# Kernel tuning notes

Measured on AMD Instinct MI355X. Metric: run time of the kernel, lower is better.

## Reference

```python
import jax, jax.numpy as jnp
import numpy as np

R_MAX = 10.0
NUM_BESSEL = 8
POLY_P = 5
EMB = 64
MLP_DIM = 256
NUM_LAYERS = 3
IN_DIM = 10
OUT_DIM = 1
N_NODES = 256
N_EDGES = 1024
N_GRAPHS = 16
# gated TP output: 0e channel carries 64 scalars + 128 gates (one per gated 1o/2e irrep)
GATE_MUL = {0: 3 * EMB, 1: EMB, 2: EMB}
L0_PATHS = [(0, 0, 0), (0, 1, 1), (0, 2, 2)]  # in_irreps = 64x0e
LN_PATHS = [(0, 0, 0), (1, 1, 0), (2, 2, 0), (0, 1, 1), (1, 0, 1), (1, 2, 1), (2, 1, 1), (0, 2, 2), (2, 0, 2), (1, 1, 2), (2, 2, 2)]

def _npaths(paths):
    d = {0: 0, 1: 0, 2: 0}
    for _, _, l3 in paths:
        d[l3] += 1
    return d

L0_NP = _npaths(L0_PATHS)
LN_NP = _npaths(LN_PATHS)
L0_NUMEL = sum(EMB * GATE_MUL[l3] for _, _, l3 in L0_PATHS)   # 20480
LN_NUMEL = sum(EMB * GATE_MUL[l3] for _, _, l3 in LN_PATHS)   # 69632

# ---- real spherical harmonics, component normalization (||Y_l||^2 = 2l+1) ----
def _sh_np(v):
    x, y, z = v[:, 0], v[:, 1], v[:, 2]
    s15 = np.sqrt(15.0)
    return {0: np.ones((v.shape[0], 1)),
            1: np.sqrt(3.0) * np.stack([x, y, z], 1),
            2: np.stack([s15 * x * y, s15 * y * z, 0.5 * np.sqrt(5.0) * (3 * z * z - 1), s15 * x * z, 0.5 * s15 * (x * x - y * y)], 1)}

def _rot(axis, t):
    c, s = np.cos(t), np.sin(t)
    R = np.eye(3)
    i, j = [(1, 2), (2, 0), (0, 1)][axis]
    R[i, i] = c; R[j, j] = c; R[i, j] = -s; R[j, i] = s
    return R

_PTS = np.random.RandomState(0).randn(64, 3)
_PTS /= np.linalg.norm(_PTS, axis=1, keepdims=True)

def _D(l, R):
    # rep matrix D with Y(Rv) = D @ Y(v), fit by least squares over sample points
    A = _sh_np(_PTS)[l]
    B = _sh_np(_PTS @ R.T)[l]
    return np.linalg.lstsq(A, B, rcond=None)[0].T

def _gen(l, axis, eps=1e-4):
    return (_D(l, _rot(axis, eps)) - _D(l, _rot(axis, -eps))) / (2 * eps)

def _cg(l1, l2, l3):
    # Clebsch-Gordan tensor as null space of the infinitesimal equivariance constraint
    d1, d2, d3 = 2 * l1 + 1, 2 * l2 + 1, 2 * l3 + 1
    rows = []
    for a in range(3):
        J1, J2, J3 = _gen(l1, a), _gen(l2, a), _gen(l3, a)
        rows.append(np.kron(J1.T, np.eye(d2 * d3)) + np.kron(np.eye(d1), np.kron(J2.T, np.eye(d3))) - np.kron(np.eye(d1 * d2), J3))
    _, _, Vh = np.linalg.svd(np.vstack(rows))
    c = Vh[-1].reshape(d1, d2, d3)
    c = c / np.linalg.norm(c)
    c = c * np.sign(c.flat[int(np.argmax(np.abs(c)))])
    return c

CG = {p: jnp.asarray(_cg(*p), jnp.float32) for p in set(LN_PATHS)}

def _sh_jax(u):
    x, y, z = u[..., 0], u[..., 1], u[..., 2]
    s15 = 15.0 ** 0.5
    return {0: jnp.ones_like(x)[:, None],
            1: (3.0 ** 0.5) * jnp.stack([x, y, z], -1),
            2: jnp.stack([s15 * x * y, s15 * y * z, 0.5 * (5.0 ** 0.5) * (3 * z * z - 1), s15 * x * z, 0.5 * s15 * (x * x - y * y)], -1)}

def _radial(r):
    # Bessel radial basis * polynomial cutoff envelope (MACE-style RadialEmbeddingBlock)
    n = jnp.arange(1, NUM_BESSEL + 1, dtype=r.dtype)
    bessel = (2.0 / R_MAX) ** 0.5 * jnp.sin(n * jnp.pi * r[:, None] / R_MAX) / r[:, None]
    x = r / R_MAX
    p = POLY_P
    env = 1.0 - 0.5 * (p + 1) * (p + 2) * x ** p + p * (p + 2) * x ** (p + 1) - 0.5 * p * (p + 1) * x ** (p + 2)
    env = env * (x < 1.0)
    return bessel * env[:, None]

def _conv(h, sh, ef, recv, send, paths, n_per, w1, b1, w2, b2):
    # TensorProductConvLayer: MLP(edge_feats) -> TP weights, CG tensor product, scatter-sum, gate
    E = ef.shape[0]
    w = jax.nn.relu(ef @ w1 + b1) @ w2 + b2  # (E, weight_numel)
    msgs = {0: 0.0, 1: 0.0, 2: 0.0}
    off = 0
    for (l1, l2, l3) in paths:
        mv = GATE_MUL[l3]
        wp = w[:, off:off + EMB * mv].reshape(E, EMB, mv)
        off += EMB * mv
        tmp = jnp.einsum('eui,ej,ijk->euk', h[l1][send], sh[l2], CG[(l1, l2, l3)])
        alpha = float(1.0 / np.sqrt(EMB * n_per[l3]))  # fan-in path normalization
        msgs[l3] = msgs[l3] + alpha * jnp.einsum('euk,euv->evk', tmp, wp)
    agg = {l: jax.ops.segment_sum(msgs[l], recv, num_segments=N_NODES) for l in msgs}
    s = agg[0][..., 0]  # (N, 192): 64 scalars + 128 gates
    return {0: jax.nn.silu(s[:, :EMB])[:, :, None],
            1: agg[1] * jax.nn.sigmoid(s[:, EMB:2 * EMB])[:, :, None],
            2: agg[2] * jax.nn.sigmoid(s[:, 2 * EMB:])[:, :, None]}

def _forward(atoms, pos, edge_index, batch, emb, l0_fc1_w, l0_fc1_b, l0_fc2_w, l0_fc2_b, fcs1_w, fcs1_b, fcs2_w, fcs2_b, pred_w1, pred_b1, pred_w2, pred_b2):
    recv, send = edge_index[0], edge_index[1]
    vec = pos[recv] - pos[send]
    r = jnp.maximum(jnp.linalg.norm(vec, axis=-1), 1e-6)
    sh = _sh_jax(vec / r[:, None])
    ef = _radial(r)
    h = {0: emb[atoms][:, :, None]}  # (N, 64, 1) scalar features
    h_new = _conv(h, sh, ef, recv, send, L0_PATHS, L0_NP, l0_fc1_w, l0_fc1_b, l0_fc2_w, l0_fc2_b)
    h_new[0] = h_new[0] + h[0]  # residual; F.pad means only scalar block overlaps
    h = h_new
    for i in range(NUM_LAYERS - 1):
        h_new = _conv(h, sh, ef, recv, send, LN_PATHS, LN_NP, fcs1_w[i], fcs1_b[i], fcs2_w[i], fcs2_b[i])
        h = {l: h_new[l] + h[l] for l in h_new}
    pooled = jax.ops.segment_sum(h[0][..., 0], batch, num_segments=N_GRAPHS)  # out[:, :emb_dim]
    return jax.nn.relu(pooled @ pred_w1 + pred_b1) @ pred_w2 + pred_b2

def setup_inputs():
    key = jax.random.key(0)
    ks = jax.random.split(key, 12)
    def lin(k, fi, fo):
        return jax.random.normal(k, (fi, fo), jnp.float32) * float(1.0 / np.sqrt(fi))
    return dict(
        atoms=jax.random.randint(ks[0], (N_NODES,), 0, IN_DIM),
        pos=jax.random.normal(ks[1], (N_NODES, 3), jnp.float32) * 2.0,
        edge_index=jax.random.randint(ks[2], (2, N_EDGES), 0, N_NODES),
        batch=jnp.sort(jax.random.randint(ks[3], (N_NODES,), 0, N_GRAPHS)),
        emb=jax.random.normal(ks[4], (IN_DIM, EMB), jnp.float32),
        l0_fc1_w=lin(ks[5], NUM_BESSEL, MLP_DIM), l0_fc1_b=jnp.zeros((MLP_DIM,), jnp.float32),
        l0_fc2_w=lin(ks[6], MLP_DIM, L0_NUMEL), l0_fc2_b=jnp.zeros((L0_NUMEL,), jnp.float32),
        fcs1_w=jax.random.normal(ks[7], (NUM_LAYERS - 1, NUM_BESSEL, MLP_DIM), jnp.float32) * float(1.0 / np.sqrt(NUM_BESSEL)),
        fcs1_b=jnp.zeros((NUM_LAYERS - 1, MLP_DIM), jnp.float32),
        fcs2_w=jax.random.normal(ks[8], (NUM_LAYERS - 1, MLP_DIM, LN_NUMEL), jnp.float32) * float(1.0 / np.sqrt(MLP_DIM)),
        fcs2_b=jnp.zeros((NUM_LAYERS - 1, LN_NUMEL), jnp.float32),
        pred_w1=lin(ks[9], EMB, EMB), pred_b1=jnp.zeros((EMB,), jnp.float32),
        pred_w2=lin(ks[10], EMB, OUT_DIM), pred_b2=jnp.zeros((OUT_DIM,), jnp.float32),
    )

def reference(atoms, pos, edge_index, batch, emb, l0_fc1_w, l0_fc1_b, l0_fc2_w, l0_fc2_b, fcs1_w, fcs1_b, fcs2_w, fcs2_b, pred_w1, pred_b1, pred_w2, pred_b2):
    return _forward(atoms, pos, edge_index, batch, emb, l0_fc1_w, l0_fc1_b, l0_fc2_w, l0_fc2_b, fcs1_w, fcs1_b, fcs2_w, fcs2_b, pred_w1, pred_b1, pred_w2, pred_b2)
```

## Files before the change

kernel.cpp:

```cpp
#include <hip/hip_runtime.h>
#include <hip/hip_bf16.h>
#include <math.h>

#define NE 1024
#define NN 256
#define NG 16
#define EMB 64
#define KD 256
#define BK 64
#define NUMEL_L0 20480
#define NUMEL_LN 69632
#define MSGW 704
#define MAXE 256

typedef __attribute__((ext_vector_type(8))) __bf16 bf16x8;
typedef __attribute__((ext_vector_type(4))) float f32x4;
typedef __attribute__((ext_vector_type(4))) unsigned int u32x4;

__device__ __align__(16) float g_sh[NE * 8];
__device__ __align__(16) float g_ef[NE * 8];
__device__ __align__(16) unsigned short g_hidb[NE * KD];
__device__ __align__(16) unsigned short g_w2t[(size_t)NUMEL_LN * KD];
__device__ __align__(16) unsigned short g_wb[(size_t)NE * NUMEL_LN];
__device__ __align__(16) float g_msgs[NE * MSGW];
__device__ __align__(16) float g_h0[NN * EMB];
__device__ __align__(16) float g_h1[NN * EMB * 3];
__device__ __align__(16) float g_h2[NN * EMB * 5];
__device__ int g_elist[NN * MAXE];
__device__ int g_ecnt[NN];
__device__ __align__(16) float g_pool[NG * EMB];
__device__ float g_cg[363];

__device__ __forceinline__ unsigned short f2b(float x) {
    __hip_bfloat16 h = __float2bfloat16(x);
    return *(unsigned short*)&h;
}
__device__ __forceinline__ float b2f(unsigned short u) {
    __hip_bfloat16 h;
    *(unsigned short*)&h = u;
    return __bfloat162float(h);
}

__device__ __forceinline__ void gld16(const void* g, void* l) {
    __builtin_amdgcn_global_load_lds(
        (const __attribute__((address_space(1))) unsigned int*)g,
        (__attribute__((address_space(3))) unsigned int*)l, 16, 0, 0);
}

struct Path { int l1, l2, d1, d2, d3, mv, off, cgoff, tmpoff; };

__constant__ Path PLN[11] = {
    {0, 0, 1, 1, 1, 192, 0,     0,   0},
    {1, 1, 3, 3, 1, 192, 12288, 1,   64},
    {2, 2, 5, 5, 1, 192, 24576, 10,  128},
    {0, 1, 1, 3, 3, 64,  36864, 35,  192},
    {1, 0, 3, 1, 3, 64,  40960, 44,  384},
    {1, 2, 3, 5, 3, 64,  45056, 53,  576},
    {2, 1, 5, 3, 3, 64,  49152, 98,  768},
    {0, 2, 1, 5, 5, 64,  53248, 143, 960},
    {2, 0, 5, 1, 5, 64,  57344, 168, 1280},
    {1, 1, 3, 3, 5, 64,  61440, 193, 1600},
    {2, 2, 5, 5, 5, 64,  65536, 238, 1920},
};
__constant__ Path PL0[3] = {
    {0, 0, 1, 1, 1, 192, 0,     0,   0},
    {0, 1, 1, 3, 3, 64,  12288, 35,  64},
    {0, 2, 1, 5, 5, 64,  16384, 143, 256},
};

__global__ void k_init_cg() {
    if (threadIdx.x != 0 || blockIdx.x != 0) return;
    for (int i = 0; i < 363; i++) g_cg[i] = 0.f;
    const float K3 = 0.57735026918962576f;
    const float K5 = 0.44721359549995794f;
    const float A  = 0.31622776601683794f;
    const float B  = 0.18257418583505536f;
    const float C2 = 0.36514837167011072f;
    const float P  = 0.23904572186687872f;
    const float Q  = 0.20701966780270626f;
    const float S  = 0.11952286093343936f;
    g_cg[0] = 1.f;
    for (int i = 0; i < 3; i++) g_cg[1 + i * 3 + i] = K3;
    for (int i = 0; i < 5; i++) g_cg[10 + i * 5 + i] = K5;
    for (int i = 0; i < 3; i++) g_cg[35 + i * 3 + i] = K3;
    for (int i = 0; i < 3; i++) g_cg[44 + i * 3 + i] = K3;
    g_cg[53 + 1]  = A;  g_cg[53 + 15] = A;  g_cg[53 + 20] = A;
    g_cg[53 + 34] = A;  g_cg[53 + 11] = A;  g_cg[53 + 39] = A;
    g_cg[53 + 6]  = -B; g_cg[53 + 22] = -B; g_cg[53 + 38] = C2;
    g_cg[53 + 12] = A;  g_cg[53 + 28] = -A;
    g_cg[98 + 1]  = A;  g_cg[98 + 3]  = A;  g_cg[98 + 14] = A;
    g_cg[98 + 16] = A;  g_cg[98 + 29] = A;  g_cg[98 + 33] = A;
    g_cg[98 + 18] = -B; g_cg[98 + 22] = -B; g_cg[98 + 26] = C2;
    g_cg[98 + 36] = A;  g_cg[98 + 40] = -A;
    for (int i = 0; i < 5; i++) g_cg[143 + i * 5 + i] = K5;
    for (int i = 0; i < 5; i++) g_cg[168 + i * 5 + i] = K5;
    g_cg[193 + 5]  = A;  g_cg[193 + 15] = A;  g_cg[193 + 26] = A;
    g_cg[193 + 36] = A;  g_cg[193 + 13] = A;  g_cg[193 + 33] = A;
    g_cg[193 + 2]  = -B; g_cg[193 + 22] = -B; g_cg[193 + 42] = C2;
    g_cg[193 + 4]  = A;  g_cg[193 + 24] = -A;
    g_cg[238 + 2]   = P;  g_cg[238 + 10]  = P;  g_cg[238 + 50]  = P;
    g_cg[238 + 8]   = -Q; g_cg[238 + 16]  = -Q; g_cg[238 + 28]  = -Q;
    g_cg[238 + 40]  = -Q; g_cg[238 + 76]  = -Q; g_cg[238 + 80]  = -Q;
    g_cg[238 + 32]  = -S; g_cg[238 + 36]  = -S; g_cg[238 + 56]  = -S;
    g_cg[238 + 34]  = Q;  g_cg[238 + 46]  = Q;  g_cg[238 + 106] = Q;
    g_cg[238 + 62]  = -P;
    g_cg[238 + 74]  = P;  g_cg[238 + 114] = P;  g_cg[238 + 122] = P;
    g_cg[238 + 68]  = -S; g_cg[238 + 88]  = -S; g_cg[238 + 92]  = -S;
    g_cg[238 + 94]  = -Q; g_cg[238 + 98]  = -Q; g_cg[238 + 118] = -Q;
}

__global__ void k_geom(const int* ei, const float* pos) {
    int e = blockIdx.x * blockDim.x + threadIdx.x;
    if (e >= NE) return;
    int recv = ei[e], send = ei[NE + e];
    float vx = pos[recv * 3 + 0] - pos[send * 3 + 0];
    float vy = pos[recv * 3 + 1] - pos[send * 3 + 1];
    float vz = pos[recv * 3 + 2] - pos[send * 3 + 2];
    float rn = sqrtf(vx * vx + vy * vy + vz * vz);
    float r = fmaxf(rn, 1e-6f);
    float x = vx / r, y = vy / r, z = vz / r;
    const float S3 = 1.7320508075688772f;
    const float S15 = 3.8729833462074170f;
    const float S5H = 1.1180339887498949f;
    const float S15H = 1.9364916731037085f;
    g_sh[e * 8 + 0] = S3 * x;
    g_sh[e * 8 + 1] = S3 * y;
    g_sh[e * 8 + 2] = S3 * z;
    g_sh[e * 8 + 3] = S15 * x * y;
    g_sh[e * 8 + 4] = S15 * y * z;
    g_sh[e * 8 + 5] = S5H * (3.f * z * z - 1.f);
    g_sh[e * 8 + 6] = S15 * x * z;
    g_sh[e * 8 + 7] = S15H * (x * x - y * y);
    float xr = r * 0.1f;
    float env = 0.f;
    if (xr < 1.f) {
        float x5 = xr * xr * xr * xr * xr;
        env = 1.f - 21.f * x5 + 35.f * x5 * xr - 15.f * x5 * xr * xr;
    }
    const float SB = 0.44721359549995794f;
    const float PI = 3.14159265358979323846f;
    for (int nb = 1; nb <= 8; nb++) {
        g_ef[e * 8 + nb - 1] = SB * sinf((float)nb * PI * r * 0.1f) / r * env;
    }
}

__global__ __launch_bounds__(256) void k_elist(const int* ei) {
    int n = blockIdx.x;
    int tid = threadIdx.x;
    int lane = tid & 63, w = tid >> 6;
    __shared__ int wsum[4];
    int mask = 0;
#pragma unroll
    for (int i = 0; i < 4; i++) {
        if (ei[tid * 4 + i] == n) mask |= 1 << i;
    }
    int nm = __popc(mask);
    int incl = nm;
#pragma unroll
    for (int off = 1; off < 64; off <<= 1) {
        int v = __shfl_up(incl, off);
        if (lane >= off) incl += v;
    }
    if (lane == 63) wsum[w] = incl;
    __syncthreads();
    int wbase = 0;
    for (int i = 0; i < w; i++) wbase += wsum[i];
    int base = wbase + incl - nm;
#pragma unroll
    for (int i = 0; i < 4; i++) {
        if (mask & (1 << i)) g_elist[n * MAXE + base++] = tid * 4 + i;
    }
    if (tid == 255) g_ecnt[n] = wbase + incl;
}

__global__ void k_inith(const int* atoms, const float* emb) {
    int idx = blockIdx.x * blockDim.x + threadIdx.x;
    if (idx >= NN * EMB) return;
    int n = idx / EMB, u = idx % EMB;
    g_h0[idx] = emb[atoms[n] * EMB + u];
    for (int k = 0; k < 3; k++) g_h1[idx * 3 + k] = 0.f;
    for (int k = 0; k < 5; k++) g_h2[idx * 5 + k] = 0.f;
}

__global__ void k_hid(const float* w1, const float* b1) {
    int e = blockIdx.x, m = threadIdx.x;
    float acc = b1[m];
    for (int nb = 0; nb < 8; nb++) acc += g_ef[e * 8 + nb] * w1[nb * KD + m];
    g_hidb[e * KD + m] = f2b(fmaxf(acc, 0.f));
}

__global__ __launch_bounds__(256) void k_w2t(const float* w2, int numel) {
    __shared__ float t[32][33];
    int n0 = blockIdx.x * 32, k0 = blockIdx.y * 32;
    int tx = threadIdx.x & 31, ty = threadIdx.x >> 5;
#pragma unroll
    for (int i = 0; i < 4; i++) {
        int kl = ty * 4 + i;
        t[kl][tx] = w2[(size_t)(k0 + kl) * numel + n0 + tx];
    }
    __syncthreads();
#pragma unroll
    for (int i = 0; i < 4; i++) {
        int nl = ty * 4 + i;
        g_w2t[(size_t)(n0 + nl) * KD + k0 + tx] = f2b(t[tx][nl]);
    }
}

__global__ __launch_bounds__(256) void k_gemm_mfma(const float* b2, int numel) {
    __shared__ unsigned short S[16384];
    int tid = threadIdx.x;
    int lane = tid & 63, wid = tid >> 6;
    int wm = wid >> 1, wn = wid & 1;
    int id = blockIdx.x;
    int xcd = id & 7;
    int q = id >> 3;
    int mb = q & 7;
    int ytile = q >> 3;
    int nt = xcd + 8 * ytile;
    int m0 = mb * 128, n0 = nt * 128;
    int fr = lane & 15;
    int ko = (lane >> 4) * 8;

    const char* gA = (const char*)g_hidb;
    const char* gB = (const char*)g_w2t;
    f32x4 acc[4][4] = {};

    for (int kst = 0; kst < 4; kst++) {
#pragma unroll
        for (int i = 0; i < 4; i++) {
            int L = wid * 4096 + i * 1024 + lane * 16;
            int row = L >> 7, p = L & 127;
            int sp = p ^ ((row & 7) << 4);
            gld16(gA + ((size_t)(m0 + row) * KD + kst * BK) * 2 + sp, (char*)S + L);
        }
#pragma unroll
        for (int i = 0; i < 4; i++) {
            int L = wid * 4096 + i * 1024 + lane * 16;
            int row = L >> 7, p = L & 127;
            int sp = p ^ ((row & 7) << 4);
            gld16(gB + ((size_t)(n0 + row) * KD + kst * BK) * 2 + sp, (char*)S + 16384 + L);
        }
        __syncthreads();
#pragma unroll
        for (int ks = 0; ks < 2; ks++) {
            int klb = ks * 64 + ko * 2;
            bf16x8 af[4], bf_[4];
#pragma unroll
            for (int f = 0; f < 4; f++) {
                int ra = wm * 64 + f * 16 + fr;
                af[f] = *(bf16x8*)((char*)S + ra * 128 + (klb ^ ((ra & 7) << 4)));
                int rb = wn * 64 + f * 16 + fr;
                bf_[f] = *(bf16x8*)((char*)S + 16384 + rb * 128 + (klb ^ ((rb & 7) << 4)));
            }
#pragma unroll
            for (int i = 0; i < 4; i++)
#pragma unroll
                for (int j = 0; j < 4; j++)
                    acc[i][j] = __builtin_amdgcn_mfma_f32_16x16x32_bf16(af[i], bf_[j], acc[i][j], 0, 0, 0);
        }
        __syncthreads();
    }

#pragma unroll
    for (int j = 0; j < 4; j++) {
        int colL = wn * 64 + j * 16 + fr;
        float bb = b2[n0 + colL];
#pragma unroll
        for (int i = 0; i < 4; i++) {
#pragma unroll
            for (int r = 0; r < 4; r++) {
                int rowL = wm * 64 + i * 16 + (lane >> 4) * 4 + r;
                *(unsigned short*)((char*)S + rowL * 256 + ((colL * 2) ^ ((rowL & 7) << 4))) =
                    f2b(acc[i][j][r] + bb);
            }
        }
    }
    __syncthreads();
    for (int c = tid; c < 2048; c += 256) {
        int row = c >> 4, p16 = (c & 15) * 16;
        u32x4 v = *(u32x4*)((char*)S + row * 256 + (p16 ^ ((row & 7) << 4)));
        *(u32x4*)((char*)(g_wb + (size_t)(m0 + row) * numel + n0) + p16) = v;
    }
}

__global__ __launch_bounds__(256) void k_contract(const int* ei, int numel, int layer0) {
    int e = blockIdx.x;
    int tid = threadIdx.x;
    __shared__ float sh[8];
    __shared__ float tmp[2240];
    __shared__ __align__(16) unsigned short wlds[64 * 192];
    int send = ei[NE + e];
    if (tid < 8) sh[tid] = g_sh[e * 8 + tid];
    __syncthreads();
    const Path* PT = layer0 ? PL0 : PLN;
    int npaths = layer0 ? 3 : 11;
    int tmptot = layer0 ? 576 : 2240;
    for (int t = tid; t < tmptot; t += 256) {
        int p = npaths - 1;
        while (t < PT[p].tmpoff) p--;
        Path pp = PT[p];
        int rem = t - pp.tmpoff;
        int u = rem / pp.d3, k = rem % pp.d3;
        float acc = 0.f;
        for (int i = 0; i < pp.d1; i++) {
            float hv = (pp.l1 == 0) ? g_h0[send * EMB + u]
                     : (pp.l1 == 1) ? g_h1[(send * EMB + u) * 3 + i]
                                    : g_h2[(send * EMB + u) * 5 + i];
            for (int j = 0; j < pp.d2; j++) {
                float sv = (pp.l2 == 0) ? 1.f : (pp.l2 == 1 ? sh[j] : sh[3 + j]);
                acc += hv * sv * g_cg[pp.cgoff + (i * pp.d2 + j) * pp.d3 + k];
            }
        }
        tmp[t] = acc;
    }
    __syncthreads();
    const unsigned short* wrow = g_wb + (size_t)e * numel;
    float alpha0 = layer0 ? 0.125f : 0.07216878364870323f;
    float alpha12 = layer0 ? 0.125f : 0.0625f;
    int g0 = layer0 ? 1 : 3, g1 = layer0 ? 2 : 7;
    float a0 = 0.f, a1 = 0.f, a2 = 0.f, a3 = 0.f, a4 = 0.f;
    for (int p = 0; p < npaths; p++) {
        Path pp = PT[p];
        if (p == 0 || p == g0 || p == g1) { a0 = a1 = a2 = a3 = a4 = 0.f; }
        {
            int cnt8 = (64 * pp.mv) >> 3;
            const bf16x8* src = (const bf16x8*)(wrow + pp.off);
            for (int c = tid; c < cnt8; c += 256)
                *(bf16x8*)&wlds[c * 8] = src[c];
        }
        __syncthreads();
        if (tid < pp.mv) {
            int to = pp.tmpoff;
            if (pp.d3 == 1) {
                for (int u = 0; u < 64; u++)
                    a0 += tmp[to + u] * b2f(wlds[u * 192 + tid]);
            } else if (pp.d3 == 3) {
                for (int u = 0; u < 64; u++) {
                    float wv = b2f(wlds[u * 64 + tid]);
                    a0 += tmp[to + u * 3 + 0] * wv;
                    a1 += tmp[to + u * 3 + 1] * wv;
                    a2 += tmp[to + u * 3 + 2] * wv;
                }
            } else {
                for (int u = 0; u < 64; u++) {
                    float wv = b2f(wlds[u * 64 + tid]);
                    a0 += tmp[to + u * 5 + 0] * wv;
                    a1 += tmp[to + u * 5 + 1] * wv;
                    a2 += tmp[to + u * 5 + 2] * wv;
                    a3 += tmp[to + u * 5 + 3] * wv;
                    a4 += tmp[to + u * 5 + 4] * wv;
                }
            }
        }
        __syncthreads();
        if (p == g0 - 1 && tid < 192) {
            g_msgs[e * MSGW + tid] = alpha0 * a0;
        }
        if (p == g1 - 1 && tid < 64) {
            g_msgs[e * MSGW + 192 + tid * 3 + 0] = alpha12 * a0;
            g_msgs[e * MSGW + 192 + tid * 3 + 1] = alpha12 * a1;
            g_msgs[e * MSGW + 192 + tid * 3 + 2] = alpha12 * a2;
        }
        if (p == npaths - 1 && tid < 64) {
            g_msgs[e * MSGW + 384 + tid * 5 + 0] = alpha12 * a0;
            g_msgs[e * MSGW + 384 + tid * 5 + 1] = alpha12 * a1;
            g_msgs[e * MSGW + 384 + tid * 5 + 2] = alpha12 * a2;
            g_msgs[e * MSGW + 384 + tid * 5 + 3] = alpha12 * a3;
            g_msgs[e * MSGW + 384 + tid * 5 + 4] = alpha12 * a4;
        }
    }
}

__global__ __launch_bounds__(256) void k_agggate() {
    int n = blockIdx.x, tid = threadIdx.x;
    __shared__ float agg[MSGW];
    int cnt = g_ecnt[n];
    for (int d = tid; d < MSGW; d += 256) {
        float a = 0.f;
        for (int idx = 0; idx < cnt; idx++) {
            int e = g_elist[n * MAXE + idx];
            a += g_msgs[e * MSGW + d];
        }
        agg[d] = a;
    }
    __syncthreads();
    if (tid < EMB) {
        int u = tid;
        float s0 = agg[u], s1 = agg[64 + u], s2 = agg[128 + u];
        float sg0 = 1.f / (1.f + expf(-s0));
        float g0 = s0 * sg0;
        float sg1 = 1.f / (1.f + expf(-s1));
        float sg2 = 1.f / (1.f + expf(-s2));
        g_h0[n * EMB + u] += g0;
        for (int k = 0; k < 3; k++) g_h1[(n * EMB + u) * 3 + k] += agg[192 + u * 3 + k] * sg1;
        for (int k = 0; k < 5; k++) g_h2[(n * EMB + u) * 5 + k] += agg[384 + u * 5 + k] * sg2;
    }
}

__global__ void k_pool(const int* batch) {
    int g = blockIdx.x, u = threadIdx.x;
    float a = 0.f;
    for (int n = 0; n < NN; n++)
        if (batch[n] == g) a += g_h0[n * EMB + u];
    g_pool[g * EMB + u] = a;
}

__global__ void k_head(const float* w1, const float* b1, const float* w2, const float* b2,
                       float* out) {
    int g = blockIdx.x, v = threadIdx.x;
    float t = b1[v];
    for (int u = 0; u < EMB; u++) t += g_pool[g * EMB + u] * w1[u * EMB + v];
    t = fmaxf(t, 0.f);
    float contrib = t * w2[v];
    for (int off = 32; off > 0; off >>= 1) contrib += __shfl_down(contrib, off);
    if (v == 0) out[g] = contrib + b2[0];
}

extern "C" void kernel_launch(void* const* d_in, const int* in_sizes, int n_in,
                              void* d_out, int out_size, void* d_ws, size_t ws_size,
                              hipStream_t stream) {
    const int* atoms = (const int*)d_in[0];
    const float* pos = (const float*)d_in[1];
    const int* ei = (const int*)d_in[2];
    const int* batch = (const int*)d_in[3];
    const float* emb = (const float*)d_in[4];
    const float* l0w1 = (const float*)d_in[5];
    const float* l0b1 = (const float*)d_in[6];
    const float* l0w2 = (const float*)d_in[7];
    const float* l0b2 = (const float*)d_in[8];
    const float* f1w = (const float*)d_in[9];
    const float* f1b = (const float*)d_in[10];
    const float* f2w = (const float*)d_in[11];
    const float* f2b = (const float*)d_in[12];
    const float* pw1 = (const float*)d_in[13];
    const float* pb1 = (const float*)d_in[14];
    const float* pw2 = (const float*)d_in[15];
    const float* pb2 = (const float*)d_in[16];
    float* out = (float*)d_out;

    k_init_cg<<<dim3(1), dim3(64), 0, stream>>>();
    k_geom<<<dim3(4), dim3(256), 0, stream>>>(ei, pos);
    k_elist<<<dim3(NN), dim3(256), 0, stream>>>(ei);
    k_inith<<<dim3(64), dim3(256), 0, stream>>>(atoms, emb);

    for (int layer = 0; layer < 3; layer++) {
        const float* w1 = layer == 0 ? l0w1 : f1w + (size_t)(layer - 1) * 8 * KD;
        const float* b1 = layer == 0 ? l0b1 : f1b + (size_t)(layer - 1) * KD;
        const float* w2 = layer == 0 ? l0w2 : f2w + (size_t)(layer - 1) * KD * NUMEL_LN;
        const float* b2 = layer == 0 ? l0b2 : f2b + (size_t)(layer - 1) * NUMEL_LN;
        int numel = layer == 0 ? NUMEL_L0 : NUMEL_LN;
        int layer0 = layer == 0 ? 1 : 0;
        k_hid<<<dim3(NE), dim3(KD), 0, stream>>>(w1, b1);
        k_w2t<<<dim3(numel / 32, 8), dim3(256), 0, stream>>>(w2, numel);
        k_gemm_mfma<<<dim3((numel / 128) * (NE / 128)), dim3(256), 0, stream>>>(b2, numel);
        k_contract<<<dim3(NE), dim3(256), 0, stream>>>(ei, numel, layer0);
        k_agggate<<<dim3(NN), dim3(256), 0, stream>>>();
    }

    k_pool<<<dim3(NG), dim3(64), 0, stream>>>(batch);
    k_head<<<dim3(NG), dim3(64), 0, stream>>>(pw1, pb1, pw2, pb2, out);
}
```

Before: 456.0 us.

## Fuse weight transpose into GEMM B-load and merge setup/pool/head kernels

The separate k_w2t pass, which transposed and converted the fp32 w2 weights to a bf16 buffer, is removed. The GEMM now reads fp32 w2 directly, converts it to bf16 and stores it swizzled into shared memory. The four setup kernels are merged into one block-dispatched k_setup launch, and pool plus head become a single block. This removes a full write and reread of the large transposed weight buffer and several launch overheads. In exchange the GEMM B-tile load becomes synchronous scalar loads instead of async global-to-LDS loads, and each weight is reread by every M tile (eight times).

```diff
diff --git a/kernel.cpp b/kernel.cpp
--- a/kernel.cpp
+++ b/kernel.cpp
@@ -20,7 +20,6 @@
 __device__ __align__(16) float g_sh[NE * 8];
 __device__ __align__(16) float g_ef[NE * 8];
 __device__ __align__(16) unsigned short g_hidb[NE * KD];
-__device__ __align__(16) unsigned short g_w2t[(size_t)NUMEL_LN * KD];
 __device__ __align__(16) unsigned short g_wb[(size_t)NE * NUMEL_LN];
 __device__ __align__(16) float g_msgs[NE * MSGW];
 __device__ __align__(16) float g_h0[NN * EMB];
@@ -28,7 +27,6 @@
 __device__ __align__(16) float g_h2[NN * EMB * 5];
 __device__ int g_elist[NN * MAXE];
 __device__ int g_ecnt[NN];
-__device__ __align__(16) float g_pool[NG * EMB];
 __device__ float g_cg[363];
 
 __device__ __forceinline__ unsigned short f2b(float x) {
@@ -68,8 +66,7 @@
     {0, 2, 1, 5, 5, 64,  16384, 143, 256},
 };
 
-__global__ void k_init_cg() {
-    if (threadIdx.x != 0 || blockIdx.x != 0) return;
+__device__ void init_cg_body() {
     for (int i = 0; i < 363; i++) g_cg[i] = 0.f;
     const float K3 = 0.57735026918962576f;
     const float K5 = 0.44721359549995794f;
@@ -109,77 +106,82 @@
     g_cg[238 + 94]  = -Q; g_cg[238 + 98]  = -Q; g_cg[238 + 118] = -Q;
 }
 
-__global__ void k_geom(const int* ei, const float* pos) {
-    int e = blockIdx.x * blockDim.x + threadIdx.x;
-    if (e >= NE) return;
-    int recv = ei[e], send = ei[NE + e];
-    float vx = pos[recv * 3 + 0] - pos[send * 3 + 0];
-    float vy = pos[recv * 3 + 1] - pos[send * 3 + 1];
-    float vz = pos[recv * 3 + 2] - pos[send * 3 + 2];
-    float rn = sqrtf(vx * vx + vy * vy + vz * vz);
-    float r = fmaxf(rn, 1e-6f);
-    float x = vx / r, y = vy / r, z = vz / r;
-    const float S3 = 1.7320508075688772f;
-    const float S15 = 3.8729833462074170f;
-    const float S5H = 1.1180339887498949f;
-    const float S15H = 1.9364916731037085f;
-    g_sh[e * 8 + 0] = S3 * x;
-    g_sh[e * 8 + 1] = S3 * y;
-    g_sh[e * 8 + 2] = S3 * z;
-    g_sh[e * 8 + 3] = S15 * x * y;
-    g_sh[e * 8 + 4] = S15 * y * z;
-    g_sh[e * 8 + 5] = S5H * (3.f * z * z - 1.f);
-    g_sh[e * 8 + 6] = S15 * x * z;
-    g_sh[e * 8 + 7] = S15H * (x * x - y * y);
-    float xr = r * 0.1f;
-    float env = 0.f;
-    if (xr < 1.f) {
-        float x5 = xr * xr * xr * xr * xr;
-        env = 1.f - 21.f * x5 + 35.f * x5 * xr - 15.f * x5 * xr * xr;
-    }
-    const float SB = 0.44721359549995794f;
-    const float PI = 3.14159265358979323846f;
-    for (int nb = 1; nb <= 8; nb++) {
-        g_ef[e * 8 + nb - 1] = SB * sinf((float)nb * PI * r * 0.1f) / r * env;
-    }
-}
-
-__global__ __launch_bounds__(256) void k_elist(const int* ei) {
-    int n = blockIdx.x;
-    int tid = threadIdx.x;
-    int lane = tid & 63, w = tid >> 6;
-    __shared__ int wsum[4];
-    int mask = 0;
-#pragma unroll
-    for (int i = 0; i < 4; i++) {
-        if (ei[tid * 4 + i] == n) mask |= 1 << i;
-    }
-    int nm = __popc(mask);
-    int incl = nm;
-#pragma unroll
-    for (int off = 1; off < 64; off <<= 1) {
-        int v = __shfl_up(incl, off);
-        if (lane >= off) incl += v;
-    }
-    if (lane == 63) wsum[w] = incl;
-    __syncthreads();
-    int wbase = 0;
-    for (int i = 0; i < w; i++) wbase += wsum[i];
-    int base = wbase + incl - nm;
-#pragma unroll
-    for (int i = 0; i < 4; i++) {
-        if (mask & (1 << i)) g_elist[n * MAXE + base++] = tid * 4 + i;
-    }
-    if (tid == 255) g_ecnt[n] = wbase + incl;
-}
-
-__global__ void k_inith(const int* atoms, const float* emb) {
-    int idx = blockIdx.x * blockDim.x + threadIdx.x;
-    if (idx >= NN * EMB) return;
-    int n = idx / EMB, u = idx % EMB;
-    g_h0[idx] = emb[atoms[n] * EMB + u];
-    for (int k = 0; k < 3; k++) g_h1[idx * 3 + k] = 0.f;
-    for (int k = 0; k < 5; k++) g_h2[idx * 5 + k] = 0.f;
+__global__ __launch_bounds__(256) void k_setup(const int* ei, const float* pos,
+                                               const int* atoms, const float* emb) {
+    int bid = blockIdx.x, tid = threadIdx.x;
+    if (bid == 0) {
+        if (tid == 0) init_cg_body();
+        return;
+    }
+    if (bid <= 4) {
+        int e = (bid - 1) * 256 + tid;
+        int recv = ei[e], send = ei[NE + e];
+        float vx = pos[recv * 3 + 0] - pos[send * 3 + 0];
+        float vy = pos[recv * 3 + 1] - pos[send * 3 + 1];
+        float vz = pos[recv * 3 + 2] - pos[send * 3 + 2];
+        float rn = sqrtf(vx * vx + vy * vy + vz * vz);
+        float r = fmaxf(rn, 1e-6f);
+        float x = vx / r, y = vy / r, z = vz / r;
+        const float S3 = 1.7320508075688772f;
+        const float S15 = 3.8729833462074170f;
+        const float S5H = 1.1180339887498949f;
+        const float S15H = 1.9364916731037085f;
+        g_sh[e * 8 + 0] = S3 * x;
+        g_sh[e * 8 + 1] = S3 * y;
+        g_sh[e * 8 + 2] = S3 * z;
+        g_sh[e * 8 + 3] = S15 * x * y;
+        g_sh[e * 8 + 4] = S15 * y * z;
+        g_sh[e * 8 + 5] = S5H * (3.f * z * z - 1.f);
+        g_sh[e * 8 + 6] = S15 * x * z;
+        g_sh[e * 8 + 7] = S15H * (x * x - y * y);
+        float xr = r * 0.1f;
+        float env = 0.f;
+        if (xr < 1.f) {
+            float x5 = xr * xr * xr * xr * xr;
+            env = 1.f - 21.f * x5 + 35.f * x5 * xr - 15.f * x5 * xr * xr;
+        }
+        const float SB = 0.44721359549995794f;
+        const float PI = 3.14159265358979323846f;
+        for (int nb = 1; nb <= 8; nb++) {
+            g_ef[e * 8 + nb - 1] = SB * sinf((float)nb * PI * r * 0.1f) / r * env;
+        }
+        return;
+    }
+    if (bid <= 68) {
+        int idx = (bid - 5) * 256 + tid;
+        int n = idx / EMB, u = idx % EMB;
+        g_h0[idx] = emb[atoms[n] * EMB + u];
+        for (int k = 0; k < 3; k++) g_h1[idx * 3 + k] = 0.f;
+        for (int k = 0; k < 5; k++) g_h2[idx * 5 + k] = 0.f;
+        return;
+    }
+    {
+        int n = bid - 69;
+        int lane = tid & 63, w = tid >> 6;
+        __shared__ int wsum[4];
+        int mask = 0;
+#pragma unroll
+        for (int i = 0; i < 4; i++) {
+            if (ei[tid * 4 + i] == n) mask |= 1 << i;
+        }
+        int nm = __popc(mask);
+        int incl = nm;
+#pragma unroll
+        for (int off = 1; off < 64; off <<= 1) {
+            int v = __shfl_up(incl, off);
+            if (lane >= off) incl += v;
+        }
+        if (lane == 63) wsum[w] = incl;
+        __syncthreads();
+        int wbase = 0;
+        for (int i = 0; i < w; i++) wbase += wsum[i];
+        int base = wbase + incl - nm;
+#pragma unroll
+        for (int i = 0; i < 4; i++) {
+            if (mask & (1 << i)) g_elist[n * MAXE + base++] = tid * 4 + i;
+        }
+        if (tid == 255) g_ecnt[n] = wbase + incl;
+    }
 }
 
 __global__ void k_hid(const float* w1, const float* b1) {
@@ -189,24 +191,7 @@
     g_hidb[e * KD + m] = f2b(fmaxf(acc, 0.f));
 }
 
-__global__ __launch_bounds__(256) void k_w2t(const float* w2, int numel) {
-    __shared__ float t[32][33];
-    int n0 = blockIdx.x * 32, k0 = blockIdx.y * 32;
-    int tx = threadIdx.x & 31, ty = threadIdx.x >> 5;
-#pragma unroll
-    for (int i = 0; i < 4; i++) {
-        int kl = ty * 4 + i;
-        t[kl][tx] = w2[(size_t)(k0 + kl) * numel + n0 + tx];
-    }
-    __syncthreads();
-#pragma unroll
-    for (int i = 0; i < 4; i++) {
-        int nl = ty * 4 + i;
-        g_w2t[(size_t)(n0 + nl) * KD + k0 + tx] = f2b(t[tx][nl]);
-    }
-}
-
-__global__ __launch_bounds__(256) void k_gemm_mfma(const float* b2, int numel) {
+__global__ __launch_bounds__(256) void k_gemm_mfma(const float* w2, const float* b2, int numel) {
     __shared__ unsigned short S[16384];
     int tid = threadIdx.x;
     int lane = tid & 63, wid = tid >> 6;
@@ -222,7 +207,6 @@
     int ko = (lane >> 4) * 8;
 
     const char* gA = (const char*)g_hidb;
-    const char* gB = (const char*)g_w2t;
     f32x4 acc[4][4] = {};
 
     for (int kst = 0; kst < 4; kst++) {
@@ -234,11 +218,14 @@
             gld16(gA + ((size_t)(m0 + row) * KD + kst * BK) * 2 + sp, (char*)S + L);
         }
 #pragma unroll
-        for (int i = 0; i < 4; i++) {
-            int L = wid * 4096 + i * 1024 + lane * 16;
-            int row = L >> 7, p = L & 127;
-            int sp = p ^ ((row & 7) << 4);
-            gld16(gB + ((size_t)(n0 + row) * KD + kst * BK) * 2 + sp, (char*)S + 16384 + L);
+        for (int pass = 0; pass < 16; pass++) {
+            int kl = pass * 4 + ((tid >> 7) << 1);
+            int n = tid & 127;
+            const float* src = w2 + (size_t)(kst * BK + kl) * numel + n0 + n;
+            float va = src[0];
+            float vb = src[numel];
+            unsigned int pk = (unsigned int)f2b(va) | ((unsigned int)f2b(vb) << 16);
+            *(unsigned int*)((char*)S + 16384 + n * 128 + ((kl * 2) ^ ((n & 7) << 4))) = pk;
         }
         __syncthreads();
 #pragma unroll
@@ -397,23 +384,22 @@
     }
 }
 
-__global__ void k_pool(const int* batch) {
-    int g = blockIdx.x, u = threadIdx.x;
+__global__ __launch_bounds__(1024) void k_poolhead(const int* batch, const float* w1,
+                                                   const float* b1, const float* w2,
+                                                   const float* b2, float* out) {
+    __shared__ float pl[NG * EMB];
+    int g = threadIdx.x >> 6, u = threadIdx.x & 63;
     float a = 0.f;
     for (int n = 0; n < NN; n++)
         if (batch[n] == g) a += g_h0[n * EMB + u];
-    g_pool[g * EMB + u] = a;
-}
-
-__global__ void k_head(const float* w1, const float* b1, const float* w2, const float* b2,
-                       float* out) {
-    int g = blockIdx.x, v = threadIdx.x;
-    float t = b1[v];
-    for (int u = 0; u < EMB; u++) t += g_pool[g * EMB + u] * w1[u * EMB + v];
+    pl[g * EMB + u] = a;
+    __syncthreads();
+    float t = b1[u];
+    for (int uu = 0; uu < EMB; uu++) t += pl[g * EMB + uu] * w1[uu * EMB + u];
     t = fmaxf(t, 0.f);
-    float contrib = t * w2[v];
+    float contrib = t * w2[u];
     for (int off = 32; off > 0; off >>= 1) contrib += __shfl_down(contrib, off);
-    if (v == 0) out[g] = contrib + b2[0];
+    if (u == 0) out[g] = contrib + b2[0];
 }
 
 extern "C" void kernel_launch(void* const* d_in, const int* in_sizes, int n_in,
@@ -438,10 +424,7 @@
     const float* pb2 = (const float*)d_in[16];
     float* out = (float*)d_out;
 
-    k_init_cg<<<dim3(1), dim3(64), 0, stream>>>();
-    k_geom<<<dim3(4), dim3(256), 0, stream>>>(ei, pos);
-    k_elist<<<dim3(NN), dim3(256), 0, stream>>>(ei);
-    k_inith<<<dim3(64), dim3(256), 0, stream>>>(atoms, emb);
+    k_setup<<<dim3(325), dim3(256), 0, stream>>>(ei, pos, atoms, emb);
 
     for (int layer = 0; layer < 3; layer++) {
         const float* w1 = layer == 0 ? l0w1 : f1w + (size_t)(layer - 1) * 8 * KD;
@@ -451,12 +434,10 @@
         int numel = layer == 0 ? NUMEL_L0 : NUMEL_LN;
         int layer0 = layer == 0 ? 1 : 0;
         k_hid<<<dim3(NE), dim3(KD), 0, stream>>>(w1, b1);
-        k_w2t<<<dim3(numel / 32, 8), dim3(256), 0, stream>>>(w2, numel);
-        k_gemm_mfma<<<dim3((numel / 128) * (NE / 128)), dim3(256), 0, stream>>>(b2, numel);
+        k_gemm_mfma<<<dim3((numel / 128) * (NE / 128)), dim3(256), 0, stream>>>(w2, b2, numel);
         k_contract<<<dim3(NE), dim3(256), 0, stream>>>(ei, numel, layer0);
         k_agggate<<<dim3(NN), dim3(256), 0, stream>>>();
     }
 
-    k_pool<<<dim3(NG), dim3(64), 0, stream>>>(batch);
-    k_head<<<dim3(NG), dim3(64), 0, stream>>>(pw1, pb1, pw2, pb2, out);
-}
+    k_poolhead<<<dim3(1), dim3(1024), 0, stream>>>(batch, pw1, pb1, pw2, pb2, out);
+}
```

Result: slower. 682.6 us (+49.7%).
